# Optimization experiments

Hardware: AMD Instinct MI355X
Metric: run time of the kernel (lower is better)

## Reference

```python
import jax, jax.numpy as jnp
import numpy as np

DIM = 768
HEADS = 8
HIDDEN = 3072
B, Hs, Ws = 16, 32, 32
N = Hs * Ws
LN_EPS = 1e-5


def setup_inputs() -> dict:
    key = jax.random.key(0)
    ks = jax.random.split(key, 10)
    s = lambda *sh: 0.02
    return {
        "x": jax.random.normal(ks[0], (B, N, DIM), jnp.float32),
        "Wq": jax.random.normal(ks[1], (DIM, DIM), jnp.float32) * 0.02,
        "temperature": jnp.ones((HEADS, 1, 1), jnp.float32),
        "fc1_w": jax.random.normal(ks[2], (HIDDEN, DIM), jnp.float32) * 0.02,
        "fc1_b": jnp.zeros((HIDDEN,), jnp.float32),
        "dw_w": jax.random.normal(ks[3], (HIDDEN, 1, 3, 3), jnp.float32) * 0.1,
        "dw_b": jnp.zeros((HIDDEN,), jnp.float32),
        "gamma": jnp.ones((HIDDEN,), jnp.float32),
        "fc2_w": jax.random.normal(ks[4], (DIM, HIDDEN), jnp.float32) * 0.02,
        "fc2_b": jnp.zeros((DIM,), jnp.float32),
        "ln_w": jnp.ones((DIM,), jnp.float32),
        "ln_b": jnp.zeros((DIM,), jnp.float32),
        "H": Hs,
        "W": Ws,
    }


def _dwconv(x, w, b, H, W):
    # x: (B, N, hidden) -> depthwise 3x3, pad 1 -> (B, N, hidden)
    Bn, Nn, Ch = x.shape
    img = x.transpose(0, 2, 1).reshape(Bn, Ch, H, W)
    out = jax.lax.conv_general_dilated(
        img, w, window_strides=(1, 1), padding=((1, 1), (1, 1)),
        dimension_numbers=("NCHW", "OIHW", "NCHW"), feature_group_count=Ch)
    out = out + b[None, :, None, None]
    return out.reshape(Bn, Ch, Nn).transpose(0, 2, 1)


def _layernorm(x, w, b):
    mu = x.mean(-1, keepdims=True)
    var = ((x - mu) ** 2).mean(-1, keepdims=True)
    return (x - mu) * jax.lax.rsqrt(var + LN_EPS) * w + b


def reference(x, Wq, temperature, fc1_w, fc1_b, dw_w, dw_b, gamma,
              fc2_w, fc2_b, ln_w, ln_b, H, W):
    # gpd_ratio == active_ratio == 1 -> pre/post scalings cancel
    Bn, Nn, C = x.shape
    h = temperature.shape[0]
    Ch = C // h
    # q/k/v heads: (B, h, N, Ch)
    q = (x @ Wq.T).reshape(Bn, Nn, h, Ch).transpose(0, 2, 1, 3)
    kv = x.reshape(Bn, Nn, h, Ch).transpose(0, 2, 1, 3)
    # channel attention: softmax over N, pool k over Ch, sigmoid gate
    qs = jax.nn.softmax(q, axis=-2).transpose(0, 1, 3, 2)      # (B,h,Ch,N)
    kp = jax.nn.softmax(kv, axis=-2).mean(-1, keepdims=True)    # (B,h,N,1)
    attn = jax.nn.sigmoid(qs @ kp) * temperature                # (B,h,Ch,1)
    # MLP on v (== x after scaling cancels): fc1 -> dwconv residual -> fc2 -> LN
    h1 = x @ fc1_w.T + fc1_b                                    # (B,N,hidden)
    h2 = gamma * _dwconv(h1, dw_w, dw_b, H, W) + h1
    v = _layernorm(h2 @ fc2_w.T + fc2_b, ln_w, ln_b)            # (B,N,C)
    v = v.reshape(Bn, Nn, h, Ch).transpose(0, 2, 1, 3)          # (B,h,N,Ch)
    prod = attn * v.transpose(0, 1, 3, 2)                       # (B,h,Ch,N)
    out = prod.transpose(0, 3, 1, 2).reshape(Bn, Nn, C)
    return out, prod.transpose(0, 1, 3, 2)
```

## Files before the change

kernel.cpp:

```cpp
#include <hip/hip_runtime.h>

#define BATCH 16
#define SEQ   1024
#define DIM   768
#define NHEAD 8
#define CHD   96
#define HID   3072
#define MTOT  (BATCH * SEQ)

using u16 = unsigned short;
typedef __attribute__((ext_vector_type(8))) short bf16x8;
typedef __attribute__((ext_vector_type(4))) float f32x4;

#define AS1 __attribute__((address_space(1)))
#define AS3 __attribute__((address_space(3)))

__device__ inline float bf2f(u16 u) {
    union { unsigned int i; float f; } v; v.i = ((unsigned int)u) << 16; return v.f;
}
__device__ inline u16 f2bf(float f) {
    union { float f; unsigned int i; } v; v.f = f;
    unsigned int r = v.i + 0x7FFFu + ((v.i >> 16) & 1u);
    return (u16)(r >> 16);
}

__device__ inline void gld16(const void* g, void* l) {
    __builtin_amdgcn_global_load_lds((AS1 const void*)g, (AS3 void*)l, 16, 0, 0);
}

template <bool HAS_BIAS>
__global__ __launch_bounds__(256) void gemm128(const u16* __restrict__ A,
                                               const u16* __restrict__ B,
                                               const float* __restrict__ bias,
                                               u16* __restrict__ C,
                                               int M, int N, int K) {
    __shared__ u16 As[128 * 64];
    __shared__ u16 Bs[128 * 64];
    const int tid = threadIdx.x;
    const int lane = tid & 63;
    const int wave = tid >> 6;
    const int wm = (wave >> 1) << 6, wn = (wave & 1) << 6;

    const int nwg = gridDim.x;
    const int wg = blockIdx.x;
    const int lid = (wg & 7) * (nwg >> 3) + (wg >> 3);
    const int nbx = N >> 7;
    const int mb = lid / nbx, nb = lid - mb * nbx;
    const int m0 = mb << 7, n0 = nb << 7;

    const int srow = tid >> 3;
    const int sce = ((tid & 7) << 3) ^ ((srow & 7) << 3);
    const u16* pa = A + (size_t)(m0 + srow) * K + sce;
    const u16* pb = B + (size_t)(n0 + srow) * K + sce;
    const size_t rstep = (size_t)32 * K;

    const int lrow = lane & 15;
    const int ksl8 = (lane >> 4) << 3;
    const int swz = (lrow & 7) << 3;
    const int c0 = ksl8 ^ swz;
    const int c1 = (32 + ksl8) ^ swz;

    f32x4 acc[4][4] = {};

    for (int k0 = 0; k0 < K; k0 += 64) {
#pragma unroll
        for (int q = 0; q < 4; ++q) {
            gld16(pa + k0 + q * rstep, &As[q * 2048 + tid * 8]);
            gld16(pb + k0 + q * rstep, &Bs[q * 2048 + tid * 8]);
        }
        __syncthreads();

        bf16x8 af[4], bf[4];
#pragma unroll
        for (int i = 0; i < 4; ++i) af[i] = *(const bf16x8*)&As[(wm + i * 16 + lrow) * 64 + c0];
#pragma unroll
        for (int j = 0; j < 4; ++j) bf[j] = *(const bf16x8*)&Bs[(wn + j * 16 + lrow) * 64 + c0];
#pragma unroll
        for (int i = 0; i < 4; ++i)
#pragma unroll
            for (int j = 0; j < 4; ++j)
                acc[i][j] = __builtin_amdgcn_mfma_f32_16x16x32_bf16(af[i], bf[j], acc[i][j], 0, 0, 0);
#pragma unroll
        for (int i = 0; i < 4; ++i) af[i] = *(const bf16x8*)&As[(wm + i * 16 + lrow) * 64 + c1];
#pragma unroll
        for (int j = 0; j < 4; ++j) bf[j] = *(const bf16x8*)&Bs[(wn + j * 16 + lrow) * 64 + c1];
#pragma unroll
        for (int i = 0; i < 4; ++i)
#pragma unroll
            for (int j = 0; j < 4; ++j)
                acc[i][j] = __builtin_amdgcn_mfma_f32_16x16x32_bf16(af[i], bf[j], acc[i][j], 0, 0, 0);
        __syncthreads();
    }

    const int crow = (lane >> 4) << 2, ccol = lane & 15;
#pragma unroll
    for (int i = 0; i < 4; ++i) {
        const int gm = m0 + wm + i * 16 + crow;
#pragma unroll
        for (int j = 0; j < 4; ++j) {
            const int gn = n0 + wn + j * 16 + ccol;
            const float bv = HAS_BIAS ? bias[gn] : 0.f;
#pragma unroll
            for (int r = 0; r < 4; ++r)
                C[(size_t)(gm + r) * N + gn] = f2bf(acc[i][j][r] + bv);
        }
    }
}

__global__ __launch_bounds__(256) void cvt_all(const float* __restrict__ x,
                                               const float* __restrict__ Wq,
                                               const float* __restrict__ w1,
                                               const float* __restrict__ w2,
                                               u16* __restrict__ xb,
                                               u16* __restrict__ Wqb,
                                               u16* __restrict__ w1b,
                                               u16* __restrict__ w2b) {
    const int E0 = MTOT * DIM / 4;
    const int E1 = E0 + DIM * DIM / 4;
    const int E2 = E1 + HID * DIM / 4;
    const int E3 = E2 + DIM * HID / 4;
    int i = blockIdx.x * 256 + threadIdx.x;
    if (i >= E3) return;
    const float* in; u16* out; int k;
    if (i < E0)      { in = x;  out = xb;  k = i; }
    else if (i < E1) { in = Wq; out = Wqb; k = i - E0; }
    else if (i < E2) { in = w1; out = w1b; k = i - E1; }
    else             { in = w2; out = w2b; k = i - E2; }
    float4 v = reinterpret_cast<const float4*>(in)[k];
    ushort4 o;
    o.x = f2bf(v.x); o.y = f2bf(v.y); o.z = f2bf(v.z); o.w = f2bf(v.w);
    reinterpret_cast<ushort4*>(out)[k] = o;
}

__global__ __launch_bounds__(256) void colsm_stats(const u16* __restrict__ X,
                                                   float* __restrict__ Mo,
                                                   float* __restrict__ So) {
    const int tid = threadIdx.x, lane = tid & 63, chunk = tid >> 6;
    const int b = blockIdx.y;
    const int j = blockIdx.x * 64 + lane;
    const u16* p = X + (size_t)b * SEQ * DIM + j;
    float m = -3.0e38f, s = 0.f;
    const int nEnd = (chunk + 1) << 8;
    for (int n = chunk << 8; n < nEnd; ++n) {
        float raw = bf2f(p[(size_t)n * DIM]);
        float nm = fmaxf(m, raw);
        s = s * __expf(m - nm) + __expf(raw - nm);
        m = nm;
    }
    __shared__ float ms[4][64], ss[4][64];
    ms[chunk][lane] = m; ss[chunk][lane] = s;
    __syncthreads();
    if (tid < 64) {
        float M = fmaxf(fmaxf(ms[0][lane], ms[1][lane]), fmaxf(ms[2][lane], ms[3][lane]));
        float S = ss[0][lane] * __expf(ms[0][lane] - M) + ss[1][lane] * __expf(ms[1][lane] - M) +
                  ss[2][lane] * __expf(ms[2][lane] - M) + ss[3][lane] * __expf(ms[3][lane] - M);
        Mo[b * DIM + j] = M;
        So[b * DIM + j] = S;
    }
}

__global__ __launch_bounds__(256) void kp_k(const u16* __restrict__ x,
                                            const float* __restrict__ Mx,
                                            const float* __restrict__ Sx,
                                            float* __restrict__ kp) {
    const int n = blockIdx.x, b = blockIdx.y, tid = threadIdx.x;
    __shared__ float p[DIM];
    const u16* row = x + ((size_t)b * SEQ + n) * DIM;
#pragma unroll
    for (int q = 0; q < 3; ++q) {
        int j = tid + (q << 8);
        p[j] = __expf(bf2f(row[j]) - Mx[b * DIM + j]) / Sx[b * DIM + j];
    }
    __syncthreads();
    if (tid < NHEAD) {
        float s = 0.f;
        for (int c = 0; c < CHD; ++c) s += p[tid * CHD + c];
        kp[((size_t)b * NHEAD + tid) * SEQ + n] = s * (1.f / (float)CHD);
    }
}

__global__ __launch_bounds__(256) void qattn_k(const u16* __restrict__ Q,
                                               const float* __restrict__ kp,
                                               const float* __restrict__ temp,
                                               float* __restrict__ attnv) {
    const int tid = threadIdx.x, lane = tid & 63, chunk = tid >> 6;
    const int b = blockIdx.y;
    const int j = blockIdx.x * 64 + lane;
    const int h = j / CHD;
    const u16* qp = Q + (size_t)b * SEQ * DIM + j;
    const float* kpp = kp + ((size_t)b * NHEAD + h) * SEQ;
    float m = -3.0e38f, s = 0.f, a = 0.f;
    const int nEnd = (chunk + 1) << 8;
    for (int n = chunk << 8; n < nEnd; ++n) {
        float q = bf2f(qp[(size_t)n * DIM]);
        float nm = fmaxf(m, q);
        float sc = __expf(m - nm), e = __expf(q - nm);
        s = s * sc + e;
        a = a * sc + e * kpp[n];
        m = nm;
    }
    __shared__ float ms[4][64], ss[4][64], as_[4][64];
    ms[chunk][lane] = m; ss[chunk][lane] = s; as_[chunk][lane] = a;
    __syncthreads();
    if (tid < 64) {
        float M = fmaxf(fmaxf(ms[0][lane], ms[1][lane]), fmaxf(ms[2][lane], ms[3][lane]));
        float S = 0.f, A = 0.f;
#pragma unroll
        for (int c = 0; c < 4; ++c) {
            float sc = __expf(ms[c][lane] - M);
            S += ss[c][lane] * sc;
            A += as_[c][lane] * sc;
        }
        float z = A / S;
        attnv[b * DIM + j] = temp[h] / (1.f + __expf(-z));
    }
}

__global__ __launch_bounds__(128) void dwconv_v(const u16* __restrict__ h1,
                                                const float* __restrict__ w,
                                                const float* __restrict__ dwb,
                                                const float* __restrict__ gamma,
                                                u16* __restrict__ h2) {
    const int g = blockIdx.x * 128 + threadIdx.x;
    const int y = blockIdx.y >> 2;
    const int xw0 = (blockIdx.y & 3) << 3;
    const int b = blockIdx.z;
    const int ch0 = g << 3;

    float wreg[8][9], bias2[8];
#pragma unroll
    for (int c = 0; c < 8; ++c) {
        const float gm = gamma[ch0 + c];
#pragma unroll
        for (int k = 0; k < 9; ++k) wreg[c][k] = gm * w[(ch0 + c) * 9 + k];
        wreg[c][4] += 1.0f;
        bias2[c] = gm * dwb[ch0 + c];
    }

    float acc[8][8];
#pragma unroll
    for (int xo = 0; xo < 8; ++xo)
#pragma unroll
        for (int c = 0; c < 8; ++c) acc[xo][c] = bias2[c];

    const u16* base = h1 + (size_t)b * SEQ * HID + ch0;
#pragma unroll
    for (int dy = 0; dy < 3; ++dy) {
        const int yy = y + dy - 1;
        if ((unsigned)yy > 31u) continue;
#pragma unroll
        for (int cr = -1; cr <= 8; ++cr) {
            const int col = xw0 + cr;
            if ((unsigned)col > 31u) continue;
            const uint4 v = *reinterpret_cast<const uint4*>(
                base + (size_t)((yy << 5) + col) * HID);
            float f[8];
            f[0] = bf2f((u16)(v.x & 0xffff)); f[1] = bf2f((u16)(v.x >> 16));
            f[2] = bf2f((u16)(v.y & 0xffff)); f[3] = bf2f((u16)(v.y >> 16));
            f[4] = bf2f((u16)(v.z & 0xffff)); f[5] = bf2f((u16)(v.z >> 16));
            f[6] = bf2f((u16)(v.w & 0xffff)); f[7] = bf2f((u16)(v.w >> 16));
            const int xlo = cr > 0 ? cr - 1 : 0;
            const int xhi = cr < 7 ? cr + 1 : 7;
#pragma unroll
            for (int xo = 0; xo < 8; ++xo) {
                if (xo < xlo || xo > xhi) continue;
                const int dx = cr - xo + 1;
#pragma unroll
                for (int c = 0; c < 8; ++c)
                    acc[xo][c] += f[c] * wreg[c][dy * 3 + dx];
            }
        }
    }

#pragma unroll
    for (int xo = 0; xo < 8; ++xo) {
        const int n = (y << 5) + xw0 + xo;
        uint4 o;
        o.x = (unsigned)f2bf(acc[xo][0]) | ((unsigned)f2bf(acc[xo][1]) << 16);
        o.y = (unsigned)f2bf(acc[xo][2]) | ((unsigned)f2bf(acc[xo][3]) << 16);
        o.z = (unsigned)f2bf(acc[xo][4]) | ((unsigned)f2bf(acc[xo][5]) << 16);
        o.w = (unsigned)f2bf(acc[xo][6]) | ((unsigned)f2bf(acc[xo][7]) << 16);
        *reinterpret_cast<uint4*>(h2 + ((size_t)b * SEQ + n) * HID + ch0) = o;
    }
}

__global__ __launch_bounds__(256) void ln_out_k(const u16* __restrict__ vpre,
                                                const float* __restrict__ lnw,
                                                const float* __restrict__ lnb,
                                                const float* __restrict__ attnv,
                                                float* __restrict__ out,
                                                float* __restrict__ out2) {
    const int n = blockIdx.x, b = blockIdx.y, tid = threadIdx.x;
    __shared__ float red[4];
    const u16* row = vpre + ((size_t)b * SEQ + n) * DIM;
    float v[3];
    float s = 0.f;
#pragma unroll
    for (int q = 0; q < 3; ++q) { v[q] = bf2f(row[tid + (q << 8)]); s += v[q]; }
#pragma unroll
    for (int o = 32; o; o >>= 1) s += __shfl_down(s, o, 64);
    if ((tid & 63) == 0) red[tid >> 6] = s;
    __syncthreads();
    const float mu = (red[0] + red[1] + red[2] + red[3]) * (1.f / (float)DIM);
    __syncthreads();
    float vs = 0.f;
#pragma unroll
    for (int q = 0; q < 3; ++q) { float d = v[q] - mu; vs += d * d; }
#pragma unroll
    for (int o = 32; o; o >>= 1) vs += __shfl_down(vs, o, 64);
    if ((tid & 63) == 0) red[tid >> 6] = vs;
    __syncthreads();
    const float rstd = rsqrtf((red[0] + red[1] + red[2] + red[3]) * (1.f / (float)DIM) + 1e-5f);
    const float* at = attnv + b * DIM;
    float* orow = out + ((size_t)b * SEQ + n) * DIM;
#pragma unroll
    for (int q = 0; q < 3; ++q) {
        int j = tid + (q << 8);
        float o = (v[q] - mu) * rstd * lnw[j] + lnb[j];
        o *= at[j];
        orow[j] = o;
        int h = j / CHD, c = j - h * CHD;
        out2[(((size_t)b * NHEAD + h) * SEQ + n) * CHD + c] = o;
    }
}

extern "C" void kernel_launch(void* const* d_in, const int* in_sizes, int n_in,
                              void* d_out, int out_size, void* d_ws, size_t ws_size,
                              hipStream_t stream) {
    const float* x     = (const float*)d_in[0];
    const float* Wq    = (const float*)d_in[1];
    const float* temp  = (const float*)d_in[2];
    const float* fc1w  = (const float*)d_in[3];
    const float* fc1b  = (const float*)d_in[4];
    const float* dww   = (const float*)d_in[5];
    const float* dwb   = (const float*)d_in[6];
    const float* gamma = (const float*)d_in[7];
    const float* fc2w  = (const float*)d_in[8];
    const float* fc2b  = (const float*)d_in[9];
    const float* lnw   = (const float*)d_in[10];
    const float* lnb   = (const float*)d_in[11];

    float* out  = (float*)d_out;
    float* out2 = out + (size_t)BATCH * SEQ * DIM;

    char* ws = (char*)d_ws;
    u16* xb     = (u16*)ws;
    u16* h1     = (u16*)(ws + 25165824);
    u16* Wqb    = (u16*)(ws + 125829120);
    u16* fc1wb  = (u16*)(ws + 127008768);
    u16* fc2wb  = (u16*)(ws + 131727360);
    float* Mx   = (float*)(ws + 136445952);
    float* Sx   = Mx + BATCH * DIM;
    float* kp   = Sx + BATCH * DIM;
    float* attnv = kp + BATCH * NHEAD * SEQ;
    u16* vpreb  = xb;

    u16* Qb = (u16*)d_out;
    u16* h2 = (u16*)d_out;

    {
        const int tot4 = (MTOT * DIM + DIM * DIM + HID * DIM + DIM * HID) / 4;
        cvt_all<<<(tot4 + 255) / 256, 256, 0, stream>>>(
            x, Wq, fc1w, fc2w, xb, Wqb, fc1wb, fc2wb);
    }

    gemm128<false><<<(MTOT / 128) * (DIM / 128), 256, 0, stream>>>(
        xb, Wqb, nullptr, Qb, MTOT, DIM, DIM);
    colsm_stats<<<dim3(DIM / 64, BATCH), 256, 0, stream>>>(xb, Mx, Sx);
    kp_k<<<dim3(SEQ, BATCH), 256, 0, stream>>>(xb, Mx, Sx, kp);
    qattn_k<<<dim3(DIM / 64, BATCH), 256, 0, stream>>>(Qb, kp, temp, attnv);

    gemm128<true><<<(MTOT / 128) * (HID / 128), 256, 0, stream>>>(
        xb, fc1wb, fc1b, h1, MTOT, HID, DIM);
    dwconv_v<<<dim3(3, 128, BATCH), 128, 0, stream>>>(h1, dww, dwb, gamma, h2);
    gemm128<true><<<(MTOT / 128) * (DIM / 128), 256, 0, stream>>>(
        h2, fc2wb, fc2b, vpreb, MTOT, DIM, HID);
    ln_out_k<<<dim3(SEQ, BATCH), 256, 0, stream>>>(vpreb, lnw, lnb, attnv, out, out2);
}
```

Before: 425.9 us.

## Pipeline GEMMs with 4-stage LDS ring and fuse Q and fc1 projections

Replaces the 128x128 single-buffered GEMM with a templated 512-thread kernel that uses a 4-slot LDS ring, explicit vmcnt waits, split A/B staging interleaved with MFMA, and setprio around the math. The Q projection and fc1 are fused into one GEMM over a concatenated weight (fc1 then Wq), with the epilogue splitting output columns into h1 (with bias) and Qb. fc2 uses a 128x256 tile. The goal is to hide global-load latency, raise MFMA utilisation and drop one launch and one extra pass over x. It relies on hand-tuned wait counts and the concatenated weight layout in the workspace being correct.

New measurement: 401.2 us. 5.8% less time.

```diff
diff --git a/kernel.cpp b/kernel.cpp
--- a/kernel.cpp
+++ b/kernel.cpp
@@ -28,81 +28,137 @@
     __builtin_amdgcn_global_load_lds((AS1 const void*)g, (AS3 void*)l, 16, 0, 0);
 }
 
-template <bool HAS_BIAS>
-__global__ __launch_bounds__(256) void gemm128(const u16* __restrict__ A,
-                                               const u16* __restrict__ B,
-                                               const float* __restrict__ bias,
-                                               u16* __restrict__ C,
-                                               int M, int N, int K) {
-    __shared__ u16 As[128 * 64];
-    __shared__ u16 Bs[128 * 64];
+template <int BM>
+__global__ __launch_bounds__(512) void gemm_p(const u16* __restrict__ A,
+                                              const u16* __restrict__ B,
+                                              const float* __restrict__ bias,
+                                              u16* __restrict__ C1, int N1,
+                                              u16* __restrict__ C2,
+                                              int M, int N, int K) {
+    constexpr int AROUNDS = BM / 128;
+    constexpr int GPT = 2 + AROUNDS;
+    constexpr int ASLOT = BM * 32;
+    constexpr int AFOLD = BM / 2;
+    constexpr int NFI = BM / 32;
+    __shared__ u16 lds[4 * (ASLOT + 8192)];
+
     const int tid = threadIdx.x;
     const int lane = tid & 63;
-    const int wave = tid >> 6;
-    const int wm = (wave >> 1) << 6, wn = (wave & 1) << 6;
+    const int wid = tid >> 6;
+    const int wm = (wid >> 2) * (BM / 2);
+    const int wn = (wid & 3) << 6;
 
     const int nwg = gridDim.x;
     const int wg = blockIdx.x;
     const int lid = (wg & 7) * (nwg >> 3) + (wg >> 3);
-    const int nbx = N >> 7;
+    const int nbx = N >> 8;
     const int mb = lid / nbx, nb = lid - mb * nbx;
-    const int m0 = mb << 7, n0 = nb << 7;
-
-    const int srow = tid >> 3;
-    const int sce = ((tid & 7) << 3) ^ ((srow & 7) << 3);
-    const u16* pa = A + (size_t)(m0 + srow) * K + sce;
-    const u16* pb = B + (size_t)(n0 + srow) * K + sce;
-    const size_t rstep = (size_t)32 * K;
+    const int m0 = mb * BM, n0 = nb << 8;
+
+    const int sprow = tid >> 3;
+    const int s_l = (tid & 7) ^ (sprow & 7);
+    const int sgk = (s_l & 3) << 3;
+    const u16* pa = A + (size_t)(m0 + (s_l >> 2) * AFOLD + sprow) * K + sgk;
+    const u16* pb = B + (size_t)(n0 + (s_l >> 2) * 128 + sprow) * K + sgk;
+    const size_t r64K = (size_t)64 * K;
+
+#define STAGE_A(slot, k0) do {                                        \
+    gld16(pa + (k0), &lds[(slot) * (ASLOT + 8192) + tid * 8]);        \
+    if (AROUNDS == 2)                                                 \
+        gld16(pa + (k0) + r64K,                                       \
+              &lds[(slot) * (ASLOT + 8192) + 4096 + tid * 8]);        \
+} while (0)
+#define STAGE_B(slot, k0) do {                                        \
+    gld16(pb + (k0), &lds[(slot) * (ASLOT + 8192) + ASLOT + tid * 8]);\
+    gld16(pb + (k0) + r64K,                                           \
+          &lds[(slot) * (ASLOT + 8192) + ASLOT + 4096 + tid * 8]);    \
+} while (0)
 
     const int lrow = lane & 15;
-    const int ksl8 = (lane >> 4) << 3;
-    const int swz = (lrow & 7) << 3;
-    const int c0 = ksl8 ^ swz;
-    const int c1 = (32 + ksl8) ^ swz;
-
-    f32x4 acc[4][4] = {};
-
-    for (int k0 = 0; k0 < K; k0 += 64) {
-#pragma unroll
-        for (int q = 0; q < 4; ++q) {
-            gld16(pa + k0 + q * rstep, &As[q * 2048 + tid * 8]);
-            gld16(pb + k0 + q * rstep, &Bs[q * 2048 + tid * 8]);
+    const int kg = lane >> 4;
+    const int xA = (((wid >> 2) * 4 + kg) ^ (lrow & 7)) << 3;
+    const int xB = (((wn >> 7) * 4 + kg) ^ (lrow & 7)) << 3;
+    const int bbase = (wn & 64) + lrow;
+
+    f32x4 acc[NFI][4] = {};
+
+    const int NT = K >> 5;
+    STAGE_A(0, 0);  STAGE_B(0, 0);
+    STAGE_A(1, 32); STAGE_B(1, 32);
+    STAGE_A(2, 64); STAGE_B(2, 64);
+
+    for (int t = 0; t < NT; ++t) {
+        const int rem = NT - 1 - t;
+        if (rem >= 2) {
+            if constexpr (GPT == 4) asm volatile("s_waitcnt vmcnt(8)" ::: "memory");
+            else                    asm volatile("s_waitcnt vmcnt(6)" ::: "memory");
+        } else if (rem == 1) {
+            if constexpr (GPT == 4) asm volatile("s_waitcnt vmcnt(4)" ::: "memory");
+            else                    asm volatile("s_waitcnt vmcnt(3)" ::: "memory");
+        } else {
+            asm volatile("s_waitcnt vmcnt(0)" ::: "memory");
         }
-        __syncthreads();
-
-        bf16x8 af[4], bf[4];
-#pragma unroll
-        for (int i = 0; i < 4; ++i) af[i] = *(const bf16x8*)&As[(wm + i * 16 + lrow) * 64 + c0];
-#pragma unroll
-        for (int j = 0; j < 4; ++j) bf[j] = *(const bf16x8*)&Bs[(wn + j * 16 + lrow) * 64 + c0];
-#pragma unroll
-        for (int i = 0; i < 4; ++i)
+        __builtin_amdgcn_sched_barrier(0);
+        __builtin_amdgcn_s_barrier();
+
+        const u16* Ls = &lds[(t & 3) * (ASLOT + 8192)];
+        const int k3 = (t + 3) << 5;
+
+        bf16x8 bfr[4], af[NFI / 2];
+#pragma unroll
+        for (int j = 0; j < 4; ++j)
+            bfr[j] = *(const bf16x8*)&Ls[ASLOT + (bbase + j * 16) * 64 + xB];
+#pragma unroll
+        for (int i = 0; i < NFI / 2; ++i)
+            af[i] = *(const bf16x8*)&Ls[(i * 16 + lrow) * 64 + xA];
+        if (rem >= 3) STAGE_A((t + 3) & 3, k3);
+        asm volatile("s_waitcnt lgkmcnt(0)" ::: "memory");
+        __builtin_amdgcn_sched_barrier(0);
+        __builtin_amdgcn_s_setprio(1);
+#pragma unroll
+        for (int i = 0; i < NFI / 2; ++i)
 #pragma unroll
             for (int j = 0; j < 4; ++j)
-                acc[i][j] = __builtin_amdgcn_mfma_f32_16x16x32_bf16(af[i], bf[j], acc[i][j], 0, 0, 0);
-#pragma unroll
-        for (int i = 0; i < 4; ++i) af[i] = *(const bf16x8*)&As[(wm + i * 16 + lrow) * 64 + c1];
-#pragma unroll
-        for (int j = 0; j < 4; ++j) bf[j] = *(const bf16x8*)&Bs[(wn + j * 16 + lrow) * 64 + c1];
-#pragma unroll
-        for (int i = 0; i < 4; ++i)
+                acc[i][j] = __builtin_amdgcn_mfma_f32_16x16x32_bf16(af[i], bfr[j], acc[i][j], 0, 0, 0);
+        __builtin_amdgcn_s_setprio(0);
+        __builtin_amdgcn_s_barrier();
+
+        bf16x8 af2[NFI / 2];
+#pragma unroll
+        for (int i = 0; i < NFI / 2; ++i)
+            af2[i] = *(const bf16x8*)&Ls[((i + NFI / 2) * 16 + lrow) * 64 + xA];
+        if (rem >= 3) STAGE_B((t + 3) & 3, k3);
+        asm volatile("s_waitcnt lgkmcnt(0)" ::: "memory");
+        __builtin_amdgcn_sched_barrier(0);
+        __builtin_amdgcn_s_setprio(1);
+#pragma unroll
+        for (int i = 0; i < NFI / 2; ++i)
 #pragma unroll
             for (int j = 0; j < 4; ++j)
-                acc[i][j] = __builtin_amdgcn_mfma_f32_16x16x32_bf16(af[i], bf[j], acc[i][j], 0, 0, 0);
-        __syncthreads();
-    }
+                acc[i + NFI / 2][j] = __builtin_amdgcn_mfma_f32_16x16x32_bf16(af2[i], bfr[j], acc[i + NFI / 2][j], 0, 0, 0);
+        __builtin_amdgcn_s_setprio(0);
+    }
+#undef STAGE_A
+#undef STAGE_B
 
     const int crow = (lane >> 4) << 2, ccol = lane & 15;
-#pragma unroll
-    for (int i = 0; i < 4; ++i) {
+    const int N2 = N - N1;
+#pragma unroll
+    for (int i = 0; i < NFI; ++i) {
         const int gm = m0 + wm + i * 16 + crow;
 #pragma unroll
         for (int j = 0; j < 4; ++j) {
             const int gn = n0 + wn + j * 16 + ccol;
-            const float bv = HAS_BIAS ? bias[gn] : 0.f;
-#pragma unroll
-            for (int r = 0; r < 4; ++r)
-                C[(size_t)(gm + r) * N + gn] = f2bf(acc[i][j][r] + bv);
+            if (gn < N1) {
+                const float bv = bias ? bias[gn] : 0.f;
+#pragma unroll
+                for (int r = 0; r < 4; ++r)
+                    C1[(size_t)(gm + r) * N1 + gn] = f2bf(acc[i][j][r] + bv);
+            } else {
+#pragma unroll
+                for (int r = 0; r < 4; ++r)
+                    C2[(size_t)(gm + r) * N2 + gn - N1] = f2bf(acc[i][j][r]);
+            }
         }
     }
 }
@@ -346,8 +402,8 @@
     char* ws = (char*)d_ws;
     u16* xb     = (u16*)ws;
     u16* h1     = (u16*)(ws + 25165824);
-    u16* Wqb    = (u16*)(ws + 125829120);
-    u16* fc1wb  = (u16*)(ws + 127008768);
+    u16* Bbig   = (u16*)(ws + 125829120);
+    u16* Wqb    = Bbig + (size_t)HID * DIM;
     u16* fc2wb  = (u16*)(ws + 131727360);
     float* Mx   = (float*)(ws + 136445952);
     float* Sx   = Mx + BATCH * DIM;
@@ -361,19 +417,18 @@
     {
         const int tot4 = (MTOT * DIM + DIM * DIM + HID * DIM + DIM * HID) / 4;
         cvt_all<<<(tot4 + 255) / 256, 256, 0, stream>>>(
-            x, Wq, fc1w, fc2w, xb, Wqb, fc1wb, fc2wb);
-    }
-
-    gemm128<false><<<(MTOT / 128) * (DIM / 128), 256, 0, stream>>>(
-        xb, Wqb, nullptr, Qb, MTOT, DIM, DIM);
+            x, Wq, fc1w, fc2w, xb, Wqb, Bbig, fc2wb);
+    }
+
+    gemm_p<256><<<(MTOT / 256) * (3840 / 256), 512, 0, stream>>>(
+        xb, Bbig, fc1b, h1, HID, Qb, MTOT, HID + DIM, DIM);
+
     colsm_stats<<<dim3(DIM / 64, BATCH), 256, 0, stream>>>(xb, Mx, Sx);
     kp_k<<<dim3(SEQ, BATCH), 256, 0, stream>>>(xb, Mx, Sx, kp);
     qattn_k<<<dim3(DIM / 64, BATCH), 256, 0, stream>>>(Qb, kp, temp, attnv);
 
-    gemm128<true><<<(MTOT / 128) * (HID / 128), 256, 0, stream>>>(
-        xb, fc1wb, fc1b, h1, MTOT, HID, DIM);
     dwconv_v<<<dim3(3, 128, BATCH), 128, 0, stream>>>(h1, dww, dwb, gamma, h2);
-    gemm128<true><<<(MTOT / 128) * (DIM / 128), 256, 0, stream>>>(
-        h2, fc2wb, fc2b, vpreb, MTOT, DIM, HID);
+    gemm_p<128><<<(MTOT / 128) * (DIM / 256), 512, 0, stream>>>(
+        h2, fc2wb, fc2b, vpreb, DIM, (u16*)nullptr, MTOT, DIM, HID);
     ln_out_k<<<dim3(SEQ, BATCH), 256, 0, stream>>>(vpreb, lnw, lnb, attnv, out, out2);
 }
```

## Fuse Q and fc1 GEMMs, shrink LDS K-tile, stage epilogue through LDS

Applied to the files above, without the earlier changes.

The Wq projection and fc1 GEMM share the same A operand (x in bf16), so their weights are laid out contiguously and computed in one 3840-wide GEMM. The epilogue splits output columns between h1 and Q, and the bias is applied only to the fc1 part. This removes a second pass over x and one launch. The GEMM K-step drops from 64 to 32, halving LDS use per block at the cost of twice as many barriers. Output tiles are now written through swizzled LDS as 16-byte coalesced stores instead of scattered 2-byte stores. Separately, kp_k replaces its shared-memory serial sum with a 32-lane shuffle reduction per head.

Result: slower. 509.0 us (+19.5%).

```diff
diff --git a/kernel.cpp b/kernel.cpp
--- a/kernel.cpp
+++ b/kernel.cpp
@@ -28,18 +28,18 @@
     __builtin_amdgcn_global_load_lds((AS1 const void*)g, (AS3 void*)l, 16, 0, 0);
 }
 
-template <bool HAS_BIAS>
 __global__ __launch_bounds__(256) void gemm128(const u16* __restrict__ A,
                                                const u16* __restrict__ B,
                                                const float* __restrict__ bias,
-                                               u16* __restrict__ C,
+                                               u16* __restrict__ C1, int N1,
+                                               u16* __restrict__ C2,
                                                int M, int N, int K) {
-    __shared__ u16 As[128 * 64];
-    __shared__ u16 Bs[128 * 64];
+    __shared__ u16 lds[8192];
     const int tid = threadIdx.x;
     const int lane = tid & 63;
     const int wave = tid >> 6;
-    const int wm = (wave >> 1) << 6, wn = (wave & 1) << 6;
+    const int wm = (wave >> 1) << 6;
+    const int wn = (wave & 1) << 6;
 
     const int nwg = gridDim.x;
     const int wg = blockIdx.x;
@@ -48,42 +48,37 @@
     const int mb = lid / nbx, nb = lid - mb * nbx;
     const int m0 = mb << 7, n0 = nb << 7;
 
-    const int srow = tid >> 3;
-    const int sce = ((tid & 7) << 3) ^ ((srow & 7) << 3);
-    const u16* pa = A + (size_t)(m0 + srow) * K + sce;
-    const u16* pb = B + (size_t)(n0 + srow) * K + sce;
-    const size_t rstep = (size_t)32 * K;
+    const int sp = tid >> 3;
+    const int sc = (tid & 7) ^ (sp & 7);
+    const int sh = sc >> 2;
+    const int skc = (sc & 3) << 3;
+    const u16* pa0 = A + (size_t)(m0 + (sh << 6) + sp) * K + skc;
+    const u16* pa1 = A + (size_t)(m0 + (sh << 6) + sp + 32) * K + skc;
+    const u16* pb0 = B + (size_t)(n0 + (sh << 6) + sp) * K + skc;
+    const u16* pb1 = B + (size_t)(n0 + (sh << 6) + sp + 32) * K + skc;
 
     const int lrow = lane & 15;
-    const int ksl8 = (lane >> 4) << 3;
-    const int swz = (lrow & 7) << 3;
-    const int c0 = ksl8 ^ swz;
-    const int c1 = (32 + ksl8) ^ swz;
+    const int kg = lane >> 4;
+    const int hA = wm >> 6, hB = wn >> 6;
+    const int offA = ((hA * 4 + kg) ^ (lrow & 7)) << 3;
+    const int offB = ((hB * 4 + kg) ^ (lrow & 7)) << 3;
 
     f32x4 acc[4][4] = {};
 
-    for (int k0 = 0; k0 < K; k0 += 64) {
-#pragma unroll
-        for (int q = 0; q < 4; ++q) {
-            gld16(pa + k0 + q * rstep, &As[q * 2048 + tid * 8]);
-            gld16(pb + k0 + q * rstep, &Bs[q * 2048 + tid * 8]);
-        }
+    for (int k0 = 0; k0 < K; k0 += 32) {
+        gld16(pa0 + k0, &lds[tid * 8]);
+        gld16(pa1 + k0, &lds[2048 + tid * 8]);
+        gld16(pb0 + k0, &lds[4096 + tid * 8]);
+        gld16(pb1 + k0, &lds[6144 + tid * 8]);
         __syncthreads();
 
         bf16x8 af[4], bf[4];
 #pragma unroll
-        for (int i = 0; i < 4; ++i) af[i] = *(const bf16x8*)&As[(wm + i * 16 + lrow) * 64 + c0];
-#pragma unroll
-        for (int j = 0; j < 4; ++j) bf[j] = *(const bf16x8*)&Bs[(wn + j * 16 + lrow) * 64 + c0];
-#pragma unroll
         for (int i = 0; i < 4; ++i)
-#pragma unroll
-            for (int j = 0; j < 4; ++j)
-                acc[i][j] = __builtin_amdgcn_mfma_f32_16x16x32_bf16(af[i], bf[j], acc[i][j], 0, 0, 0);
-#pragma unroll
-        for (int i = 0; i < 4; ++i) af[i] = *(const bf16x8*)&As[(wm + i * 16 + lrow) * 64 + c1];
-#pragma unroll
-        for (int j = 0; j < 4; ++j) bf[j] = *(const bf16x8*)&Bs[(wn + j * 16 + lrow) * 64 + c1];
+            af[i] = *(const bf16x8*)&lds[(i * 16 + lrow) * 64 + offA];
+#pragma unroll
+        for (int j = 0; j < 4; ++j)
+            bf[j] = *(const bf16x8*)&lds[4096 + (j * 16 + lrow) * 64 + offB];
 #pragma unroll
         for (int i = 0; i < 4; ++i)
 #pragma unroll
@@ -93,17 +88,37 @@
     }
 
     const int crow = (lane >> 4) << 2, ccol = lane & 15;
-#pragma unroll
-    for (int i = 0; i < 4; ++i) {
-        const int gm = m0 + wm + i * 16 + crow;
-#pragma unroll
-        for (int j = 0; j < 4; ++j) {
-            const int gn = n0 + wn + j * 16 + ccol;
-            const float bv = HAS_BIAS ? bias[gn] : 0.f;
-#pragma unroll
-            for (int r = 0; r < 4; ++r)
-                C[(size_t)(gm + r) * N + gn] = f2bf(acc[i][j][r] + bv);
+    const int N2 = N - N1;
+#pragma unroll
+    for (int p = 0; p < 2; ++p) {
+        if ((wave >> 1) == p) {
+#pragma unroll
+            for (int i = 0; i < 4; ++i) {
+#pragma unroll
+                for (int j = 0; j < 4; ++j) {
+                    const int col = wn + j * 16 + ccol;
+                    const int gn = n0 + col;
+                    const float bv = (gn < N1 && bias) ? bias[gn] : 0.f;
+#pragma unroll
+                    for (int r = 0; r < 4; ++r) {
+                        const int lr = i * 16 + crow + r;
+                        lds[lr * 128 + (((col >> 3) ^ (lr & 7)) << 3) + (col & 7)] =
+                            f2bf(acc[i][j][r] + bv);
+                    }
+                }
+            }
         }
+        __syncthreads();
+#pragma unroll
+        for (int k = 0; k < 4; ++k) {
+            const int c = tid + (k << 8);
+            const int row = c >> 4, s = c & 15;
+            bf16x8 v = *(const bf16x8*)&lds[row * 128 + ((s ^ (row & 7)) << 3)];
+            const int gm = m0 + p * 64 + row, gnb = n0 + (s << 3);
+            if (gnb < N1) *(bf16x8*)&C1[(size_t)gm * N1 + gnb] = v;
+            else          *(bf16x8*)&C2[(size_t)gm * N2 + gnb - N1] = v;
+        }
+        __syncthreads();
     }
 }
 
@@ -164,19 +179,19 @@
                                             const float* __restrict__ Sx,
                                             float* __restrict__ kp) {
     const int n = blockIdx.x, b = blockIdx.y, tid = threadIdx.x;
-    __shared__ float p[DIM];
     const u16* row = x + ((size_t)b * SEQ + n) * DIM;
+    const int h = tid >> 5, c0 = tid & 31;
+    const float* Mrow = Mx + b * DIM;
+    const float* Srow = Sx + b * DIM;
+    float s = 0.f;
 #pragma unroll
     for (int q = 0; q < 3; ++q) {
-        int j = tid + (q << 8);
-        p[j] = __expf(bf2f(row[j]) - Mx[b * DIM + j]) / Sx[b * DIM + j];
-    }
-    __syncthreads();
-    if (tid < NHEAD) {
-        float s = 0.f;
-        for (int c = 0; c < CHD; ++c) s += p[tid * CHD + c];
-        kp[((size_t)b * NHEAD + tid) * SEQ + n] = s * (1.f / (float)CHD);
-    }
+        const int j = h * CHD + c0 + (q << 5);
+        s += __expf(bf2f(row[j]) - Mrow[j]) / Srow[j];
+    }
+#pragma unroll
+    for (int o = 16; o; o >>= 1) s += __shfl_down(s, o, 32);
+    if (c0 == 0) kp[((size_t)b * NHEAD + h) * SEQ + n] = s * (1.f / (float)CHD);
 }
 
 __global__ __launch_bounds__(256) void qattn_k(const u16* __restrict__ Q,
@@ -346,8 +361,8 @@
     char* ws = (char*)d_ws;
     u16* xb     = (u16*)ws;
     u16* h1     = (u16*)(ws + 25165824);
-    u16* Wqb    = (u16*)(ws + 125829120);
-    u16* fc1wb  = (u16*)(ws + 127008768);
+    u16* Bbig   = (u16*)(ws + 125829120);
+    u16* Wqb    = Bbig + (size_t)HID * DIM;
     u16* fc2wb  = (u16*)(ws + 131727360);
     float* Mx   = (float*)(ws + 136445952);
     float* Sx   = Mx + BATCH * DIM;
@@ -361,19 +376,18 @@
     {
         const int tot4 = (MTOT * DIM + DIM * DIM + HID * DIM + DIM * HID) / 4;
         cvt_all<<<(tot4 + 255) / 256, 256, 0, stream>>>(
-            x, Wq, fc1w, fc2w, xb, Wqb, fc1wb, fc2wb);
-    }
-
-    gemm128<false><<<(MTOT / 128) * (DIM / 128), 256, 0, stream>>>(
-        xb, Wqb, nullptr, Qb, MTOT, DIM, DIM);
+            x, Wq, fc1w, fc2w, xb, Wqb, Bbig, fc2wb);
+    }
+
+    gemm128<<<(MTOT / 128) * (3840 / 128), 256, 0, stream>>>(
+        xb, Bbig, fc1b, h1, HID, Qb, MTOT, HID + DIM, DIM);
+
     colsm_stats<<<dim3(DIM / 64, BATCH), 256, 0, stream>>>(xb, Mx, Sx);
     kp_k<<<dim3(SEQ, BATCH), 256, 0, stream>>>(xb, Mx, Sx, kp);
     qattn_k<<<dim3(DIM / 64, BATCH), 256, 0, stream>>>(Qb, kp, temp, attnv);
 
-    gemm128<true><<<(MTOT / 128) * (HID / 128), 256, 0, stream>>>(
-        xb, fc1wb, fc1b, h1, MTOT, HID, DIM);
     dwconv_v<<<dim3(3, 128, BATCH), 128, 0, stream>>>(h1, dww, dwb, gamma, h2);
-    gemm128<true><<<(MTOT / 128) * (DIM / 128), 256, 0, stream>>>(
-        h2, fc2wb, fc2b, vpreb, MTOT, DIM, HID);
+    gemm128<<<(MTOT / 128) * (DIM / 128), 256, 0, stream>>>(
+        h2, fc2wb, fc2b, vpreb, DIM, (u16*)nullptr, MTOT, DIM, HID);
     ln_out_k<<<dim3(SEQ, BATCH), 256, 0, stream>>>(vpreb, lnw, lnb, attnv, out, out2);
 }
```
